# Kernel tuning notes

Measured on AMD Instinct MI355X. Metric: run time of the kernel, lower is better.

Reference implementation:

```python
import jax, jax.numpy as jnp
import numpy as np

EPS = 1e-8
LN_EPS = 1e-5

def _normalize(x):
    # torch F.normalize: x / max(||x||_2, eps)
    n = jnp.linalg.norm(x, axis=-1, keepdims=True)
    return x / jnp.maximum(n, EPS)

def _gelu(x):
    return jax.nn.gelu(x, approximate=False)

def _layernorm(x, g, b):
    mu = jnp.mean(x, axis=-1, keepdims=True)
    var = jnp.var(x, axis=-1, keepdims=True)
    return (x - mu) / jnp.sqrt(var + LN_EPS) * g + b

def setup_inputs() -> dict:
    B, M, N, D = 128, 256, 1024, 256
    key = jax.random.key(0)
    ks = jax.random.split(key, 10)
    def lin(k, fi, fo):
        kw, kb = jax.random.split(k)
        lim = 1.0 / np.sqrt(fi)
        W = jax.random.uniform(kw, (fi, fo), minval=-lim, maxval=lim, dtype=jnp.float32)
        b = jax.random.uniform(kb, (fo,), minval=-lim, maxval=lim, dtype=jnp.float32)
        return W, b
    Wg1, bg1 = lin(ks[0], D, D)
    Wg2, bg2 = lin(ks[1], D, 1)
    Wo1, bo1 = lin(ks[2], 2 * D, D)
    Wo2, bo2 = lin(ks[3], D, D)
    Ws1, bs1 = lin(ks[4], D, D // 2)
    Ws2, bs2 = lin(ks[5], D // 2, 1)
    return {
        "visual_tokens": jax.random.normal(ks[6], (B, N, D), dtype=jnp.float32),
        "text_tokens": jax.random.normal(ks[7], (B, M, D), dtype=jnp.float32),
        "text_mask": jax.random.randint(ks[8], (B, M), 0, 2, dtype=jnp.int32),
        "Wg1": Wg1, "bg1": bg1, "Wg2": Wg2, "bg2": bg2,
        "Wo1": Wo1, "bo1": bo1, "ln_g": jnp.ones((D,), jnp.float32), "ln_b": jnp.zeros((D,), jnp.float32),
        "Wo2": Wo2, "bo2": bo2,
        "Ws1": Ws1, "bs1": bs1, "Ws2": Ws2, "bs2": bs2,
    }

def reference(visual_tokens, text_tokens, text_mask,
              Wg1, bg1, Wg2, bg2, Wo1, bo1, ln_g, ln_b, Wo2, bo2,
              Ws1, bs1, Ws2, bs2):
    vis = _normalize(visual_tokens)   # [B,N,D]
    txt = _normalize(text_tokens)     # [B,M,D]
    sim = jnp.einsum('bmd,bnd->bmn', txt, vis)           # token_patch_sim [B,M,N]
    token_maxsim = jnp.max(sim, axis=-1)                 # [B,M]
    token_best_patch_idx = jnp.argmax(sim, axis=-1)      # [B,M] int
    gathered = jnp.take_along_axis(vis, token_best_patch_idx[..., None], axis=1)  # [B,M,D]
    pair = jnp.concatenate([txt, gathered], axis=-1)     # [B,M,2D]
    # out_proj: Linear -> LayerNorm -> GELU -> Linear
    pair = _gelu(_layernorm(pair @ Wo1 + bo1, ln_g, ln_b)) @ Wo2 + bo2  # [B,M,D]
    # token_gate: Linear -> GELU -> Linear(D,1)
    gate = (_gelu(pair @ Wg1 + bg1) @ Wg2 + bg2)[..., 0]  # [B,M]
    mask = text_mask.astype(sim.dtype)
    token_maxsim = jnp.where(mask == 0, 0.0, token_maxsim)
    gate = jnp.where(mask == 0, -10000.0, gate)
    sim = jnp.where(mask[..., None] == 0, -1.0, sim)
    w = jax.nn.softmax(gate, axis=-1)
    w = w * mask
    w = w / jnp.maximum(jnp.sum(w, axis=-1, keepdims=True), EPS)
    grounding = jnp.sum(pair * w[..., None], axis=1)                   # [B,D]
    contradiction = 1.0 - jnp.sum(token_maxsim * w, axis=-1, keepdims=True)  # [B,1]
    patch_attn = jax.nn.softmax(jnp.swapaxes(sim, 1, 2), axis=-1)      # [B,N,M]
    weighted_patch = jnp.einsum('bnm,bmd->bnd', patch_attn, txt)       # [B,N,D]
    feat = grounding * contradiction + grounding
    score = jax.nn.sigmoid(_gelu(feat @ Ws1 + bs1) @ Ws2 + bs2)        # [B,1]
    pf = jnp.clip(token_maxsim, 0.0, 1.0)
    token_logits = jnp.stack([1.0 - pf, pf], axis=-1)                  # [B,M,2]
    return (sim, token_maxsim, token_best_patch_idx, token_logits,
            grounding, score, weighted_patch)
```

## Files before the change

kernel.cpp:

```cpp
#include <hip/hip_runtime.h>
#include <math.h>

static constexpr int Bc = 128;
static constexpr int Mc = 256;
static constexpr int Nc = 1024;
static constexpr int Dc = 256;

typedef __attribute__((ext_vector_type(8))) short bfrag;
typedef __attribute__((ext_vector_type(4))) float f32x4;

__device__ __forceinline__ float gelu_exact(float x) {
    return 0.5f * x * (1.0f + erff(x * 0.70710678118654752440f));
}

__device__ __forceinline__ unsigned short f2bf_rne(float x) {
    unsigned u = __builtin_bit_cast(unsigned, x);
    unsigned r = u + 0x7fffu + ((u >> 16) & 1u);
    return (unsigned short)(r >> 16);
}
__device__ __forceinline__ unsigned pk2(unsigned short a, unsigned short b) {
    return (unsigned)a | ((unsigned)b << 16);
}

__global__ void normalize_k(const float* __restrict__ vis,
                            const float* __restrict__ txt,
                            unsigned short* __restrict__ vis_b,
                            unsigned short* __restrict__ txt_b,
                            float* __restrict__ invv,
                            float* __restrict__ invt) {
    int wave = (blockIdx.x * blockDim.x + threadIdx.x) >> 6;
    int lane = threadIdx.x & 63;
    const int visRows = Bc * Nc;
    const float* src; unsigned short* dst; float* invp; long long row;
    if (wave < visRows) { src = vis; dst = vis_b; invp = invv; row = wave; }
    else { src = txt; dst = txt_b; invp = invt; row = wave - visRows; }
    float4 v = ((const float4*)(src + row * Dc))[lane];
    float ss = v.x * v.x + v.y * v.y + v.z * v.z + v.w * v.w;
    #pragma unroll
    for (int off = 32; off; off >>= 1) ss += __shfl_xor(ss, off);
    float sc = 1.0f / fmaxf(sqrtf(ss), 1e-8f);
    if (lane == 0) invp[row] = sc;
    unsigned short h0 = f2bf_rne(v.x * sc), h1 = f2bf_rne(v.y * sc);
    unsigned short h2 = f2bf_rne(v.z * sc), h3 = f2bf_rne(v.w * sc);
    *(uint2*)(dst + row * 256 + lane * 4) = make_uint2(pk2(h0, h1), pk2(h2, h3));
}

__global__ __launch_bounds__(256) void tcvt(const float* __restrict__ W,
                                            unsigned short* __restrict__ Wt,
                                            int R, int Cdim) {
    __shared__ unsigned short T[64 * 72];
    int r0 = blockIdx.x * 64, c0 = blockIdx.y * 64;
    int t = threadIdx.x;
    int rl = t >> 4, c4 = (t & 15) << 2;
    #pragma unroll
    for (int i = 0; i < 4; i++) {
        int r = rl + i * 16;
        float4 v = *(const float4*)(W + (long long)(r0 + r) * Cdim + c0 + c4);
        T[(c4 + 0) * 72 + r] = f2bf_rne(v.x);
        T[(c4 + 1) * 72 + r] = f2bf_rne(v.y);
        T[(c4 + 2) * 72 + r] = f2bf_rne(v.z);
        T[(c4 + 3) * 72 + r] = f2bf_rne(v.w);
    }
    __syncthreads();
    #pragma unroll
    for (int i = 0; i < 2; i++) {
        int cc = i * 256 + t, cl = cc >> 3, seg = cc & 7;
        unsigned short sv[8];
        #pragma unroll
        for (int j = 0; j < 8; j++) sv[j] = T[cl * 72 + seg * 8 + j];
        *(uint4*)(Wt + (long long)(c0 + cl) * R + r0 + seg * 8) = *(uint4*)sv;
    }
}

__global__ __launch_bounds__(256) void t_txt(const unsigned short* __restrict__ txt_b,
                                             unsigned short* __restrict__ Tt) {
    __shared__ unsigned short T[64 * 72];
    int b = blockIdx.z;
    int m0 = blockIdx.x * 64, d0 = blockIdx.y * 64;
    const unsigned short* in = txt_b + (long long)b * 256 * 256;
    unsigned short* out = Tt + (long long)b * 256 * 256;
    int t = threadIdx.x;
    #pragma unroll
    for (int i = 0; i < 2; i++) {
        int cc = i * 256 + t, ml = cc >> 3, seg = cc & 7;
        uint4 v = *(const uint4*)(in + (long long)(m0 + ml) * 256 + d0 + seg * 8);
        unsigned short sv[8];
        *(uint4*)sv = v;
        #pragma unroll
        for (int j = 0; j < 8; j++) T[(seg * 8 + j) * 72 + ml] = sv[j];
    }
    __syncthreads();
    #pragma unroll
    for (int i = 0; i < 2; i++) {
        int cc = i * 256 + t, dl = cc >> 3, seg = cc & 7;
        unsigned short sv[8];
        #pragma unroll
        for (int j = 0; j < 8; j++) sv[j] = T[dl * 72 + seg * 8 + j];
        *(uint4*)(out + (long long)(d0 + dl) * 256 + m0 + seg * 8) = *(uint4*)sv;
    }
}

template <int EPI>
__global__ __launch_bounds__(256) void gemm_nt(const unsigned short* __restrict__ A,
                                               const unsigned short* __restrict__ B,
                                               const float* __restrict__ bias,
                                               float* __restrict__ C,
                                               unsigned short* __restrict__ Cs,
                                               int Ks, int lda, int ldb, int ldc,
                                               long long sA, long long sB, long long sC) {
    __shared__ unsigned short As[128 * 64];
    __shared__ unsigned short Bs[128 * 64];
    int z = blockIdx.z;
    const unsigned short* Ab = A + (long long)z * sA + (long long)blockIdx.y * 128 * lda;
    const unsigned short* Bb = B + (long long)z * sB + (long long)blockIdx.x * 128 * ldb;
    int t = threadIdx.x;
    int lane = t & 63, wid = t >> 6;
    int wr = wid >> 1, wc = wid & 1;
    int lr = lane & 15, lk = lane >> 4;
    f32x4 acc[4][4];
    #pragma unroll
    for (int i = 0; i < 4; i++)
        #pragma unroll
        for (int j = 0; j < 4; j++) acc[i][j] = (f32x4){0.f, 0.f, 0.f, 0.f};

    for (int k0 = 0; k0 < Ks; k0 += 64) {
        uint4 va[4], vb[4];
        #pragma unroll
        for (int i = 0; i < 4; i++) {
            int c = i * 256 + t, row = c >> 3, kc = c & 7;
            va[i] = *(const uint4*)(Ab + (long long)row * lda + k0 + kc * 8);
            vb[i] = *(const uint4*)(Bb + (long long)row * ldb + k0 + kc * 8);
        }
        __syncthreads();
        #pragma unroll
        for (int i = 0; i < 4; i++) {
            int c = i * 256 + t, row = c >> 3, kc = c & 7;
            int dst = row * 64 + ((kc ^ (row & 7)) << 3);
            *(uint4*)(As + dst) = va[i];
            *(uint4*)(Bs + dst) = vb[i];
        }
        __syncthreads();
        #pragma unroll
        for (int ks = 0; ks < 2; ks++) {
            bfrag av[4], bv[4];
            #pragma unroll
            for (int f = 0; f < 4; f++) {
                int ra = wr * 64 + f * 16 + lr;
                av[f] = *(const bfrag*)(As + ra * 64 + ((((ks << 2) | lk) ^ (ra & 7)) << 3));
                int rb = wc * 64 + f * 16 + lr;
                bv[f] = *(const bfrag*)(Bs + rb * 64 + ((((ks << 2) | lk) ^ (rb & 7)) << 3));
            }
            #pragma unroll
            for (int fm = 0; fm < 4; fm++)
                #pragma unroll
                for (int fn = 0; fn < 4; fn++)
                    acc[fm][fn] = __builtin_amdgcn_mfma_f32_16x16x32_bf16(av[fm], bv[fn], acc[fm][fn], 0, 0, 0);
        }
    }

    long long cb = (long long)z * sC;
    int rbase = blockIdx.y * 128 + wr * 64;
    int cbase = blockIdx.x * 128 + wc * 64;
    #pragma unroll
    for (int fn = 0; fn < 4; fn++) {
        int col = cbase + fn * 16 + lr;
        float bv_ = (EPI > 0) ? bias[col] : 0.0f;
        #pragma unroll
        for (int fm = 0; fm < 4; fm++) {
            #pragma unroll
            for (int r = 0; r < 4; r++) {
                int row = rbase + fm * 16 + lk * 4 + r;
                float v = acc[fm][fn][r] + bv_;
                if (EPI == 3) v = gelu_exact(v);
                C[cb + (long long)row * ldc + col] = v;
                if (EPI == 2) Cs[(long long)row * ldc + col] = f2bf_rne(v);
            }
        }
    }
}

__global__ void rowstats_kernel(float* __restrict__ sim,
                                const int* __restrict__ mask,
                                const float* __restrict__ txt,
                                const float* __restrict__ vis,
                                const float* __restrict__ invt,
                                const float* __restrict__ invv,
                                float* __restrict__ tms_out,
                                float* __restrict__ idx_out,
                                float* __restrict__ logits_out,
                                int* __restrict__ idx_ws) {
    __shared__ int candS[4][64];
    __shared__ int cntS[4];
    int w = threadIdx.x >> 6, lane = threadIdx.x & 63;
    int row = blockIdx.x * 4 + w;
    float* srow = sim + (long long)row * Nc;
    float4 vals[4];
    float best = -3.0e38f;
    #pragma unroll
    for (int s = 0; s < 4; s++) {
        vals[s] = *(const float4*)(srow + s * 256 + lane * 4);
        best = fmaxf(best, fmaxf(fmaxf(vals[s].x, vals[s].y), fmaxf(vals[s].z, vals[s].w)));
    }
    #pragma unroll
    for (int off = 32; off; off >>= 1) best = fmaxf(best, __shfl_xor(best, off));
    if (lane == 0) cntS[w] = 0;
    __syncthreads();
    float th = best - 4e-3f;
    #pragma unroll
    for (int s = 0; s < 4; s++) {
        int base = s * 256 + lane * 4;
        float4 v = vals[s];
        if (v.x >= th) { int sl = atomicAdd(&cntS[w], 1); if (sl < 64) candS[w][sl] = base; }
        if (v.y >= th) { int sl = atomicAdd(&cntS[w], 1); if (sl < 64) candS[w][sl] = base + 1; }
        if (v.z >= th) { int sl = atomicAdd(&cntS[w], 1); if (sl < 64) candS[w][sl] = base + 2; }
        if (v.w >= th) { int sl = atomicAdd(&cntS[w], 1); if (sl < 64) candS[w][sl] = base + 3; }
    }
    __syncthreads();
    int cnt = min(cntS[w], 64);
    int b = row >> 8;
    int bi = candS[w][0];
    if (cnt > 1) {
        float4 t4 = ((const float4*)(txt + (long long)row * Dc))[lane];
        float it = invt[row];
        float bestv = -3.0e38f; bi = 1 << 30;
        for (int c = 0; c < cnt; c++) {
            int n = candS[w][c];
            float4 v4 = ((const float4*)(vis + ((long long)b * Nc + n) * Dc))[lane];
            float d = t4.x * v4.x + t4.y * v4.y + t4.z * v4.z + t4.w * v4.w;
            #pragma unroll
            for (int off = 32; off; off >>= 1) d += __shfl_xor(d, off);
            float val = d * it * invv[b * Nc + n];
            if (val > bestv || (val == bestv && n < bi)) { bestv = val; bi = n; }
        }
    }
    int mk = mask[row];
    if (lane == 0) {
        float tms = mk ? best : 0.0f;
        tms_out[row] = tms;
        idx_out[row] = (float)bi;
        idx_ws[row] = bi;
        float pf = fminf(fmaxf(tms, 0.0f), 1.0f);
        logits_out[row * 2 + 0] = 1.0f - pf;
        logits_out[row * 2 + 1] = pf;
    }
    if (mk == 0) {
        float4 mv = make_float4(-1.0f, -1.0f, -1.0f, -1.0f);
        #pragma unroll
        for (int s = 0; s < 4; s++) *(float4*)(srow + s * 256 + lane * 4) = mv;
    }
}

__global__ void colstats_kernel(const float* __restrict__ sim,
                                float* __restrict__ cmax,
                                float* __restrict__ crecip) {
    int b = blockIdx.y;
    int n = blockIdx.x * 256 + threadIdx.x;
    const float* base = sim + (long long)b * Mc * Nc + n;
    float mx = -3.0e38f;
    for (int m = 0; m < Mc; m++) mx = fmaxf(mx, base[(long long)m * Nc]);
    float s = 0.0f;
    for (int m = 0; m < Mc; m++) s += expf(base[(long long)m * Nc] - mx);
    cmax[b * Nc + n] = mx;
    crecip[b * Nc + n] = 1.0f / s;
}

__global__ __launch_bounds__(256) void wp_gemm(const float* __restrict__ sim,
                                               const unsigned short* __restrict__ Tt,
                                               const float* __restrict__ cmax,
                                               const float* __restrict__ crecip,
                                               float* __restrict__ wpout) {
    __shared__ unsigned short As[128 * 64];
    __shared__ unsigned short Bs[128 * 64];
    int z = blockIdx.z;
    const float* S = sim + (long long)z * Mc * Nc;
    const unsigned short* Bb = Tt + (long long)z * 256 * 256 + (long long)blockIdx.x * 128 * 256;
    int n0 = blockIdx.y * 128;
    int t = threadIdx.x;
    int lane = t & 63, wid = t >> 6, wr = wid >> 1, wc = wid & 1;
    int lr = lane & 15, lk = lane >> 4;
    int nl = t & 127, mh = t >> 7;
    float cm = cmax[(long long)z * Nc + n0 + nl];
    float cr = crecip[(long long)z * Nc + n0 + nl];
    f32x4 acc[4][4];
    #pragma unroll
    for (int i = 0; i < 4; i++)
        #pragma unroll
        for (int j = 0; j < 4; j++) acc[i][j] = (f32x4){0.f, 0.f, 0.f, 0.f};

    for (int g = 0; g < 4; g++) {
        uint4 vb[4];
        #pragma unroll
        for (int i = 0; i < 4; i++) {
            int c = i * 256 + t, row = c >> 3, kc = c & 7;
            vb[i] = *(const uint4*)(Bb + (long long)row * 256 + g * 64 + kc * 8);
        }
        unsigned short pv[32];
        #pragma unroll
        for (int j = 0; j < 32; j++) {
            int m = g * 64 + mh * 32 + j;
            float v = S[(long long)m * Nc + n0 + nl];
            pv[j] = f2bf_rne(expf(v - cm) * cr);
        }
        __syncthreads();
        #pragma unroll
        for (int i = 0; i < 4; i++) {
            int c = i * 256 + t, row = c >> 3, kc = c & 7;
            *(uint4*)(Bs + row * 64 + ((kc ^ (row & 7)) << 3)) = vb[i];
        }
        #pragma unroll
        for (int q = 0; q < 4; q++) {
            uint4 h = make_uint4(pk2(pv[q * 8 + 0], pv[q * 8 + 1]), pk2(pv[q * 8 + 2], pv[q * 8 + 3]),
                                 pk2(pv[q * 8 + 4], pv[q * 8 + 5]), pk2(pv[q * 8 + 6], pv[q * 8 + 7]));
            *(uint4*)(As + nl * 64 + (((mh * 4 + q) ^ (nl & 7)) << 3)) = h;
        }
        __syncthreads();
        #pragma unroll
        for (int ks = 0; ks < 2; ks++) {
            bfrag av[4], bv2[4];
            #pragma unroll
            for (int f = 0; f < 4; f++) {
                int ra = wr * 64 + f * 16 + lr;
                av[f] = *(const bfrag*)(As + ra * 64 + ((((ks << 2) | lk) ^ (ra & 7)) << 3));
                int rb = wc * 64 + f * 16 + lr;
                bv2[f] = *(const bfrag*)(Bs + rb * 64 + ((((ks << 2) | lk) ^ (rb & 7)) << 3));
            }
            #pragma unroll
            for (int fm = 0; fm < 4; fm++)
                #pragma unroll
                for (int fn = 0; fn < 4; fn++)
                    acc[fm][fn] = __builtin_amdgcn_mfma_f32_16x16x32_bf16(av[fm], bv2[fn], acc[fm][fn], 0, 0, 0);
        }
        __syncthreads();
    }

    float* C = wpout + (long long)z * Nc * Dc;
    int rbase = n0 + wr * 64;
    int cbase = blockIdx.x * 128 + wc * 64;
    #pragma unroll
    for (int fn = 0; fn < 4; fn++) {
        int col = cbase + fn * 16 + lr;
        #pragma unroll
        for (int fm = 0; fm < 4; fm++) {
            #pragma unroll
            for (int r = 0; r < 4; r++) {
                int row = rbase + fm * 16 + lk * 4 + r;
                C[(long long)row * Dc + col] = acc[fm][fn][r];
            }
        }
    }
}

__global__ void gatherpair_k(const unsigned short* __restrict__ txt_b,
                             const unsigned short* __restrict__ vis_b,
                             const int* __restrict__ idx_ws,
                             unsigned short* __restrict__ pair_b) {
    int wave = (blockIdx.x * blockDim.x + threadIdx.x) >> 6;
    int lane = threadIdx.x & 63;
    int b = wave >> 8;
    int bi = idx_ws[wave];
    int half = lane >> 5, c = lane & 31;
    const unsigned short* srcrow = half ? (vis_b + ((long long)b * Nc + bi) * 256)
                                        : (txt_b + (long long)wave * 256);
    uint4 v = *(const uint4*)(srcrow + c * 8);
    *(uint4*)(pair_b + (long long)wave * 512 + half * 256 + c * 8) = v;
}

__global__ void lngelu_k(const float* __restrict__ H,
                         unsigned short* __restrict__ Hb,
                         const float* __restrict__ g,
                         const float* __restrict__ bta) {
    int wave = (blockIdx.x * blockDim.x + threadIdx.x) >> 6;
    int lane = threadIdx.x & 63;
    float4 v = ((const float4*)(H + (long long)wave * Dc))[lane];
    float s = v.x + v.y + v.z + v.w;
    #pragma unroll
    for (int off = 32; off; off >>= 1) s += __shfl_xor(s, off);
    float mu = s * (1.0f / 256.0f);
    float dx = v.x - mu, dy = v.y - mu, dz = v.z - mu, dw = v.w - mu;
    float ss = dx * dx + dy * dy + dz * dz + dw * dw;
    #pragma unroll
    for (int off = 32; off; off >>= 1) ss += __shfl_xor(ss, off);
    float rstd = 1.0f / sqrtf(ss * (1.0f / 256.0f) + 1e-5f);
    float4 G4 = ((const float4*)g)[lane];
    float4 B4 = ((const float4*)bta)[lane];
    unsigned short h0 = f2bf_rne(gelu_exact(dx * rstd * G4.x + B4.x));
    unsigned short h1 = f2bf_rne(gelu_exact(dy * rstd * G4.y + B4.y));
    unsigned short h2 = f2bf_rne(gelu_exact(dz * rstd * G4.z + B4.z));
    unsigned short h3 = f2bf_rne(gelu_exact(dw * rstd * G4.w + B4.w));
    *(uint2*)(Hb + (long long)wave * 256 + lane * 4) = make_uint2(pk2(h0, h1), pk2(h2, h3));
}

__global__ void gate_kernel(const float* __restrict__ G,
                            const float* __restrict__ Wg2,
                            const float* __restrict__ bg2,
                            float* __restrict__ gate) {
    int wave = (blockIdx.x * blockDim.x + threadIdx.x) >> 6;
    int lane = threadIdx.x & 63;
    float4 v = ((const float4*)(G + (long long)wave * Dc))[lane];
    float4 w = ((const float4*)Wg2)[lane];
    float s = v.x * w.x + v.y * w.y + v.z * w.z + v.w * w.w;
    #pragma unroll
    for (int off = 32; off; off >>= 1) s += __shfl_xor(s, off);
    if (lane == 0) gate[wave] = s + bg2[0];
}

__global__ __launch_bounds__(256) void final_kernel(const float* __restrict__ gate,
                                                    const int* __restrict__ mask,
                                                    const float* __restrict__ tms,
                                                    const float* __restrict__ pairO,
                                                    const float* __restrict__ Ws1,
                                                    const float* __restrict__ bs1,
                                                    const float* __restrict__ Ws2,
                                                    const float* __restrict__ bs2,
                                                    float* __restrict__ grounding_out,
                                                    float* __restrict__ score_out) {
    __shared__ float wS[256];
    __shared__ float featS[256];
    __shared__ float hS[128];
    __shared__ float red4[4];
    int b = blockIdx.x, t = threadIdx.x;
    int mk = mask[b * Mc + t];
    float g = mk ? gate[b * Mc + t] : -10000.0f;

    float mx = g;
    #pragma unroll
    for (int off = 32; off; off >>= 1) mx = fmaxf(mx, __shfl_xor(mx, off));
    if ((t & 63) == 0) red4[t >> 6] = mx;
    __syncthreads();
    mx = fmaxf(fmaxf(red4[0], red4[1]), fmaxf(red4[2], red4[3]));
    __syncthreads();

    float e = expf(g - mx);
    float ssum = e;
    #pragma unroll
    for (int off = 32; off; off >>= 1) ssum += __shfl_xor(ssum, off);
    if ((t & 63) == 0) red4[t >> 6] = ssum;
    __syncthreads();
    ssum = red4[0] + red4[1] + red4[2] + red4[3];
    __syncthreads();

    float w = (e / ssum) * (float)mk;
    float s2 = w;
    #pragma unroll
    for (int off = 32; off; off >>= 1) s2 += __shfl_xor(s2, off);
    if ((t & 63) == 0) red4[t >> 6] = s2;
    __syncthreads();
    s2 = red4[0] + red4[1] + red4[2] + red4[3];
    __syncthreads();
    w = w / fmaxf(s2, 1e-8f);
    wS[t] = w;

    float cpart = tms[b * Mc + t] * w;
    #pragma unroll
    for (int off = 32; off; off >>= 1) cpart += __shfl_xor(cpart, off);
    if ((t & 63) == 0) red4[t >> 6] = cpart;
    __syncthreads();
    float contra = 1.0f - (red4[0] + red4[1] + red4[2] + red4[3]);
    __syncthreads();

    const float* P = pairO + (long long)b * Mc * Dc;
    float acc = 0.0f;
    for (int m = 0; m < Mc; m++) acc += wS[m] * P[(long long)m * Dc + t];
    grounding_out[b * Dc + t] = acc;
    featS[t] = acc * (1.0f + contra);
    __syncthreads();

    if (t < 128) {
        float a = bs1[t];
        for (int k = 0; k < Dc; k++) a += featS[k] * Ws1[k * 128 + t];
        hS[t] = gelu_exact(a) * Ws2[t];
    }
    __syncthreads();
    if (t == 0) {
        float sc = bs2[0];
        for (int k = 0; k < 128; k++) sc += hS[k];
        score_out[b] = 1.0f / (1.0f + expf(-sc));
    }
}

extern "C" void kernel_launch(void* const* d_in, const int* in_sizes, int n_in,
                              void* d_out, int out_size, void* d_ws, size_t ws_size,
                              hipStream_t stream) {
    const float* vis  = (const float*)d_in[0];
    const float* txt  = (const float*)d_in[1];
    const int*   mask = (const int*)d_in[2];
    const float* Wg1  = (const float*)d_in[3];
    const float* bg1  = (const float*)d_in[4];
    const float* Wg2  = (const float*)d_in[5];
    const float* bg2  = (const float*)d_in[6];
    const float* Wo1  = (const float*)d_in[7];
    const float* bo1  = (const float*)d_in[8];
    const float* ln_g = (const float*)d_in[9];
    const float* ln_b = (const float*)d_in[10];
    const float* Wo2  = (const float*)d_in[11];
    const float* bo2  = (const float*)d_in[12];
    const float* Ws1  = (const float*)d_in[13];
    const float* bs1  = (const float*)d_in[14];
    const float* Ws2  = (const float*)d_in[15];
    const float* bs2  = (const float*)d_in[16];

    float* out = (float*)d_out;
    float* o_sim    = out;
    float* o_tms    = o_sim + (size_t)Bc * Mc * Nc;
    float* o_idx    = o_tms + (size_t)Bc * Mc;
    float* o_logits = o_idx + (size_t)Bc * Mc;
    float* o_ground = o_logits + (size_t)Bc * Mc * 2;
    float* o_score  = o_ground + (size_t)Bc * Dc;
    float* o_wp     = o_score + (size_t)Bc;

    char* wsb = (char*)d_ws;
    unsigned short* vis_b  = (unsigned short*)(wsb + 0);
    unsigned short* txt_b  = (unsigned short*)(wsb + 67108864);
    unsigned short* Tt     = (unsigned short*)(wsb + 83886080);
    unsigned short* pair_b = (unsigned short*)(wsb + 100663296);
    float*          H1     = (float*)(wsb + 134217728);
    unsigned short* H1_b   = (unsigned short*)(wsb + 167772160);
    float*          pairO  = (float*)(wsb + 184549376);
    unsigned short* pairO_b= (unsigned short*)(wsb + 218103808);
    float*          Gb     = (float*)(wsb + 234881024);
    char* sm = wsb + 268435456;
    float* invv    = (float*)(sm + 0);
    float* invt    = (float*)(sm + 524288);
    float* cmaxb   = (float*)(sm + 655360);
    float* crecipb = (float*)(sm + 1179648);
    int*   idx_ws  = (int*)(sm + 1703936);
    float* gateb   = (float*)(sm + 1835008);
    unsigned short* Wo1_t = (unsigned short*)(sm + 1966080);
    unsigned short* Wo2_t = (unsigned short*)(sm + 2228224);
    unsigned short* Wg1_t = (unsigned short*)(sm + 2359296);

    normalize_k<<<(Bc * Nc + Bc * Mc) / 4, 256, 0, stream>>>(vis, txt, vis_b, txt_b, invv, invt);
    tcvt<<<dim3(8, 4), 256, 0, stream>>>(Wo1, Wo1_t, 512, 256);
    tcvt<<<dim3(4, 4), 256, 0, stream>>>(Wo2, Wo2_t, 256, 256);
    tcvt<<<dim3(4, 4), 256, 0, stream>>>(Wg1, Wg1_t, 256, 256);
    gemm_nt<0><<<dim3(8, 2, 128), 256, 0, stream>>>(txt_b, vis_b, nullptr, o_sim, nullptr,
                                                    256, 256, 256, 1024,
                                                    256LL * 256, 1024LL * 256, 256LL * 1024);
    rowstats_kernel<<<(Bc * Mc) / 4, 256, 0, stream>>>(o_sim, mask, txt, vis, invt, invv,
                                                       o_tms, o_idx, o_logits, idx_ws);
    colstats_kernel<<<dim3(Nc / 256, Bc), 256, 0, stream>>>(o_sim, cmaxb, crecipb);
    t_txt<<<dim3(4, 4, 128), 256, 0, stream>>>(txt_b, Tt);
    wp_gemm<<<dim3(2, 8, 128), 256, 0, stream>>>(o_sim, Tt, cmaxb, crecipb, o_wp);
    gatherpair_k<<<(Bc * Mc) / 4, 256, 0, stream>>>(txt_b, vis_b, idx_ws, pair_b);
    gemm_nt<1><<<dim3(2, 256, 1), 256, 0, stream>>>(pair_b, Wo1_t, bo1, H1, nullptr,
                                                    512, 512, 512, 256, 0, 0, 0);
    lngelu_k<<<(Bc * Mc) / 4, 256, 0, stream>>>(H1, H1_b, ln_g, ln_b);
    gemm_nt<2><<<dim3(2, 256, 1), 256, 0, stream>>>(H1_b, Wo2_t, bo2, pairO, pairO_b,
                                                    256, 256, 256, 256, 0, 0, 0);
    gemm_nt<3><<<dim3(2, 256, 1), 256, 0, stream>>>(pairO_b, Wg1_t, bg1, Gb, nullptr,
                                                    256, 256, 256, 256, 0, 0, 0);
    gate_kernel<<<(Bc * Mc) / 4, 256, 0, stream>>>(Gb, Wg2, bg2, gateb);
    final_kernel<<<Bc, 256, 0, stream>>>(gateb, mask, o_tms, pairO, Ws1, bs1, Ws2, bs2, o_ground, o_score);
}
```

Baseline: 887.5 us.

## Fuse gate projection into GEMM epilogue, use direct-to-LDS loads, restructure stats kernels

Merges the three weight-transpose launches and the gate bias init into one prep kernel. The gate GEMM epilogue now applies GELU, dots with Wg2 and atomically adds into the gate buffer, which removes the Gb intermediate and the gate_kernel pass. GEMM tile loads switch to global_load_lds with swizzled source addresses. Column stats become a single-pass online softmax with float4 loads, wp_gemm covers all 256 output columns per block with 512 threads, and the final kernel runs 512 threads to split its reductions. The atomics make gate summation order nondeterministic.

Result: faster. 753.6 us (-15.1%).

```diff
diff --git a/kernel.cpp b/kernel.cpp
--- a/kernel.cpp
+++ b/kernel.cpp
@@ -20,6 +20,13 @@
 }
 __device__ __forceinline__ unsigned pk2(unsigned short a, unsigned short b) {
     return (unsigned)a | ((unsigned)b << 16);
+}
+
+__device__ __forceinline__ void gld16(const unsigned short* g, unsigned short* l) {
+    __builtin_amdgcn_global_load_lds(
+        (const __attribute__((address_space(1))) unsigned int*)g,
+        (__attribute__((address_space(3))) unsigned int*)l,
+        16, 0, 0);
 }
 
 __global__ void normalize_k(const float* __restrict__ vis,
@@ -45,11 +52,10 @@
     *(uint2*)(dst + row * 256 + lane * 4) = make_uint2(pk2(h0, h1), pk2(h2, h3));
 }
 
-__global__ __launch_bounds__(256) void tcvt(const float* __restrict__ W,
-                                            unsigned short* __restrict__ Wt,
-                                            int R, int Cdim) {
-    __shared__ unsigned short T[64 * 72];
-    int r0 = blockIdx.x * 64, c0 = blockIdx.y * 64;
+__device__ __forceinline__ void tile_tcvt(const float* W, unsigned short* Wt,
+                                          int R, int Cdim, int rt, int ct,
+                                          unsigned short* T) {
+    int r0 = rt * 64, c0 = ct * 64;
     int t = threadIdx.x;
     int rl = t >> 4, c4 = (t & 15) << 2;
     #pragma unroll
@@ -69,6 +75,27 @@
         #pragma unroll
         for (int j = 0; j < 8; j++) sv[j] = T[cl * 72 + seg * 8 + j];
         *(uint4*)(Wt + (long long)(c0 + cl) * R + r0 + seg * 8) = *(uint4*)sv;
+    }
+}
+
+__global__ __launch_bounds__(256) void prep_k(const float* __restrict__ Wo1,
+                                              const float* __restrict__ Wo2,
+                                              const float* __restrict__ Wg1,
+                                              unsigned short* __restrict__ Wo1_t,
+                                              unsigned short* __restrict__ Wo2_t,
+                                              unsigned short* __restrict__ Wg1_t,
+                                              const float* __restrict__ bg2,
+                                              float* __restrict__ gateb) {
+    __shared__ unsigned short T[64 * 72];
+    int job = blockIdx.x;
+    if (job < 32)      tile_tcvt(Wo1, Wo1_t, 512, 256, job >> 2, job & 3, T);
+    else if (job < 48) tile_tcvt(Wo2, Wo2_t, 256, 256, (job - 32) >> 2, (job - 32) & 3, T);
+    else if (job < 64) tile_tcvt(Wg1, Wg1_t, 256, 256, (job - 48) >> 2, (job - 48) & 3, T);
+    else {
+        float v = bg2[0];
+        int base = (job - 64) * 8192 + threadIdx.x;
+        #pragma unroll
+        for (int i = 0; i < 32; i++) gateb[base + i * 256] = v;
     }
 }
 
@@ -106,6 +133,8 @@
                                                const float* __restrict__ bias,
                                                float* __restrict__ C,
                                                unsigned short* __restrict__ Cs,
+                                               const float* __restrict__ wg2,
+                                               float* __restrict__ gateo,
                                                int Ks, int lda, int ldb, int ldc,
                                                long long sA, long long sB, long long sC) {
     __shared__ unsigned short As[128 * 64];
@@ -124,20 +153,15 @@
         for (int j = 0; j < 4; j++) acc[i][j] = (f32x4){0.f, 0.f, 0.f, 0.f};
 
     for (int k0 = 0; k0 < Ks; k0 += 64) {
-        uint4 va[4], vb[4];
+        __syncthreads();
         #pragma unroll
         for (int i = 0; i < 4; i++) {
-            int c = i * 256 + t, row = c >> 3, kc = c & 7;
-            va[i] = *(const uint4*)(Ab + (long long)row * lda + k0 + kc * 8);
-            vb[i] = *(const uint4*)(Bb + (long long)row * ldb + k0 + kc * 8);
-        }
-        __syncthreads();
-        #pragma unroll
-        for (int i = 0; i < 4; i++) {
-            int c = i * 256 + t, row = c >> 3, kc = c & 7;
-            int dst = row * 64 + ((kc ^ (row & 7)) << 3);
-            *(uint4*)(As + dst) = va[i];
-            *(uint4*)(Bs + dst) = vb[i];
+            int wb = i * 256 + (t & 192);
+            int c  = wb + (t & 63);
+            int row = c >> 3, p = c & 7;
+            int sw = (p ^ (row & 7)) << 3;
+            gld16(Ab + (long long)row * lda + k0 + sw, As + wb * 8);
+            gld16(Bb + (long long)row * ldb + k0 + sw, Bs + wb * 8);
         }
         __syncthreads();
         #pragma unroll
@@ -158,22 +182,46 @@
         }
     }
 
-    long long cb = (long long)z * sC;
     int rbase = blockIdx.y * 128 + wr * 64;
     int cbase = blockIdx.x * 128 + wc * 64;
-    #pragma unroll
-    for (int fn = 0; fn < 4; fn++) {
-        int col = cbase + fn * 16 + lr;
-        float bv_ = (EPI > 0) ? bias[col] : 0.0f;
-        #pragma unroll
-        for (int fm = 0; fm < 4; fm++) {
+    if constexpr (EPI == 4) {
+        float part[4][4] = {};
+        #pragma unroll
+        for (int fn = 0; fn < 4; fn++) {
+            int col = cbase + fn * 16 + lr;
+            float bv_ = bias[col];
+            float w2 = wg2[col];
+            #pragma unroll
+            for (int fm = 0; fm < 4; fm++)
+                #pragma unroll
+                for (int r = 0; r < 4; r++)
+                    part[fm][r] += gelu_exact(acc[fm][fn][r] + bv_) * w2;
+        }
+        #pragma unroll
+        for (int fm = 0; fm < 4; fm++)
             #pragma unroll
             for (int r = 0; r < 4; r++) {
-                int row = rbase + fm * 16 + lk * 4 + r;
-                float v = acc[fm][fn][r] + bv_;
-                if (EPI == 3) v = gelu_exact(v);
-                C[cb + (long long)row * ldc + col] = v;
-                if (EPI == 2) Cs[(long long)row * ldc + col] = f2bf_rne(v);
+                float p = part[fm][r];
+                p += __shfl_xor(p, 1); p += __shfl_xor(p, 2);
+                p += __shfl_xor(p, 4); p += __shfl_xor(p, 8);
+                if (lr == 0) atomicAdd(&gateo[rbase + fm * 16 + lk * 4 + r], p);
+            }
+    } else {
+        long long cb = (long long)z * sC;
+        #pragma unroll
+        for (int fn = 0; fn < 4; fn++) {
+            int col = cbase + fn * 16 + lr;
+            float bv_ = (EPI > 0) ? bias[col] : 0.0f;
+            #pragma unroll
+            for (int fm = 0; fm < 4; fm++) {
+                #pragma unroll
+                for (int r = 0; r < 4; r++) {
+                    int row = rbase + fm * 16 + lk * 4 + r;
+                    float v = acc[fm][fn][r] + bv_;
+                    if (EPI == 3) v = gelu_exact(v);
+                    C[cb + (long long)row * ldc + col] = v;
+                    if (EPI == 2) Cs[(long long)row * ldc + col] = f2bf_rne(v);
+                }
             }
         }
     }
@@ -250,33 +298,40 @@
     }
 }
 
-__global__ void colstats_kernel(const float* __restrict__ sim,
-                                float* __restrict__ cmax,
-                                float* __restrict__ crecip) {
+__global__ __launch_bounds__(128) void colstats_kernel(const float* __restrict__ sim,
+                                                       float* __restrict__ cmax,
+                                                       float* __restrict__ crecip) {
     int b = blockIdx.y;
-    int n = blockIdx.x * 256 + threadIdx.x;
-    const float* base = sim + (long long)b * Mc * Nc + n;
-    float mx = -3.0e38f;
-    for (int m = 0; m < Mc; m++) mx = fmaxf(mx, base[(long long)m * Nc]);
-    float s = 0.0f;
-    for (int m = 0; m < Mc; m++) s += expf(base[(long long)m * Nc] - mx);
-    cmax[b * Nc + n] = mx;
-    crecip[b * Nc + n] = 1.0f / s;
-}
-
-__global__ __launch_bounds__(256) void wp_gemm(const float* __restrict__ sim,
+    int n4 = (blockIdx.x * 128 + threadIdx.x) * 4;
+    const float* base = sim + (long long)b * Mc * Nc + n4;
+    float4 mx = make_float4(-3.0e38f, -3.0e38f, -3.0e38f, -3.0e38f);
+    float4 s = make_float4(0.f, 0.f, 0.f, 0.f);
+    for (int m = 0; m < Mc; m++) {
+        float4 v = *(const float4*)(base + (long long)m * Nc);
+        float nm;
+        nm = fmaxf(mx.x, v.x); s.x = s.x * expf(mx.x - nm) + expf(v.x - nm); mx.x = nm;
+        nm = fmaxf(mx.y, v.y); s.y = s.y * expf(mx.y - nm) + expf(v.y - nm); mx.y = nm;
+        nm = fmaxf(mx.z, v.z); s.z = s.z * expf(mx.z - nm) + expf(v.z - nm); mx.z = nm;
+        nm = fmaxf(mx.w, v.w); s.w = s.w * expf(mx.w - nm) + expf(v.w - nm); mx.w = nm;
+    }
+    *(float4*)(cmax + b * Nc + n4) = mx;
+    *(float4*)(crecip + b * Nc + n4) = make_float4(1.f / s.x, 1.f / s.y, 1.f / s.z, 1.f / s.w);
+}
+
+__global__ __launch_bounds__(512) void wp_gemm(const float* __restrict__ sim,
                                                const unsigned short* __restrict__ Tt,
                                                const float* __restrict__ cmax,
                                                const float* __restrict__ crecip,
                                                float* __restrict__ wpout) {
     __shared__ unsigned short As[128 * 64];
-    __shared__ unsigned short Bs[128 * 64];
-    int z = blockIdx.z;
+    __shared__ unsigned short Bs[256 * 64];
+    int z = blockIdx.y;
+    int n0 = blockIdx.x * 128;
     const float* S = sim + (long long)z * Mc * Nc;
-    const unsigned short* Bb = Tt + (long long)z * 256 * 256 + (long long)blockIdx.x * 128 * 256;
-    int n0 = blockIdx.y * 128;
+    const unsigned short* Bb = Tt + (long long)z * 256 * 256;
     int t = threadIdx.x;
-    int lane = t & 63, wid = t >> 6, wr = wid >> 1, wc = wid & 1;
+    int lane = t & 63, wid = t >> 6;
+    int wr = wid >> 2, wc = wid & 3;
     int lr = lane & 15, lk = lane >> 4;
     int nl = t & 127, mh = t >> 7;
     float cm = cmax[(long long)z * Nc + n0 + nl];
@@ -288,30 +343,27 @@
         for (int j = 0; j < 4; j++) acc[i][j] = (f32x4){0.f, 0.f, 0.f, 0.f};
 
     for (int g = 0; g < 4; g++) {
-        uint4 vb[4];
-        #pragma unroll
-        for (int i = 0; i < 4; i++) {
-            int c = i * 256 + t, row = c >> 3, kc = c & 7;
-            vb[i] = *(const uint4*)(Bb + (long long)row * 256 + g * 64 + kc * 8);
-        }
-        unsigned short pv[32];
-        #pragma unroll
-        for (int j = 0; j < 32; j++) {
-            int m = g * 64 + mh * 32 + j;
+        unsigned short pv[16];
+        #pragma unroll
+        for (int j = 0; j < 16; j++) {
+            int m = g * 64 + mh * 16 + j;
             float v = S[(long long)m * Nc + n0 + nl];
             pv[j] = f2bf_rne(expf(v - cm) * cr);
         }
         __syncthreads();
         #pragma unroll
         for (int i = 0; i < 4; i++) {
-            int c = i * 256 + t, row = c >> 3, kc = c & 7;
-            *(uint4*)(Bs + row * 64 + ((kc ^ (row & 7)) << 3)) = vb[i];
-        }
-        #pragma unroll
-        for (int q = 0; q < 4; q++) {
+            int wb = i * 512 + (t & 448);
+            int c  = wb + (t & 63);
+            int row = c >> 3, p = c & 7;
+            gld16(Bb + (long long)row * 256 + g * 64 + ((p ^ (row & 7)) << 3), Bs + wb * 8);
+        }
+        #pragma unroll
+        for (int q = 0; q < 2; q++) {
+            int chunk = mh * 2 + q;
             uint4 h = make_uint4(pk2(pv[q * 8 + 0], pv[q * 8 + 1]), pk2(pv[q * 8 + 2], pv[q * 8 + 3]),
                                  pk2(pv[q * 8 + 4], pv[q * 8 + 5]), pk2(pv[q * 8 + 6], pv[q * 8 + 7]));
-            *(uint4*)(As + nl * 64 + (((mh * 4 + q) ^ (nl & 7)) << 3)) = h;
+            *(uint4*)(As + nl * 64 + ((chunk ^ (nl & 7)) << 3)) = h;
         }
         __syncthreads();
         #pragma unroll
@@ -330,12 +382,11 @@
                 for (int fn = 0; fn < 4; fn++)
                     acc[fm][fn] = __builtin_amdgcn_mfma_f32_16x16x32_bf16(av[fm], bv2[fn], acc[fm][fn], 0, 0, 0);
         }
-        __syncthreads();
     }
 
     float* C = wpout + (long long)z * Nc * Dc;
     int rbase = n0 + wr * 64;
-    int cbase = blockIdx.x * 128 + wc * 64;
+    int cbase = wc * 64;
     #pragma unroll
     for (int fn = 0; fn < 4; fn++) {
         int col = cbase + fn * 16 + lr;
@@ -390,21 +441,7 @@
     *(uint2*)(Hb + (long long)wave * 256 + lane * 4) = make_uint2(pk2(h0, h1), pk2(h2, h3));
 }
 
-__global__ void gate_kernel(const float* __restrict__ G,
-                            const float* __restrict__ Wg2,
-                            const float* __restrict__ bg2,
-                            float* __restrict__ gate) {
-    int wave = (blockIdx.x * blockDim.x + threadIdx.x) >> 6;
-    int lane = threadIdx.x & 63;
-    float4 v = ((const float4*)(G + (long long)wave * Dc))[lane];
-    float4 w = ((const float4*)Wg2)[lane];
-    float s = v.x * w.x + v.y * w.y + v.z * w.z + v.w * w.w;
-    #pragma unroll
-    for (int off = 32; off; off >>= 1) s += __shfl_xor(s, off);
-    if (lane == 0) gate[wave] = s + bg2[0];
-}
-
-__global__ __launch_bounds__(256) void final_kernel(const float* __restrict__ gate,
+__global__ __launch_bounds__(512) void final_kernel(const float* __restrict__ gate,
                                                     const int* __restrict__ mask,
                                                     const float* __restrict__ tms,
                                                     const float* __restrict__ pairO,
@@ -418,63 +455,93 @@
     __shared__ float featS[256];
     __shared__ float hS[128];
     __shared__ float red4[4];
+    __shared__ float gpart[512];
+    __shared__ float hpart[512];
+    __shared__ float contraS;
     int b = blockIdx.x, t = threadIdx.x;
-    int mk = mask[b * Mc + t];
-    float g = mk ? gate[b * Mc + t] : -10000.0f;
-
-    float mx = g;
-    #pragma unroll
-    for (int off = 32; off; off >>= 1) mx = fmaxf(mx, __shfl_xor(mx, off));
-    if ((t & 63) == 0) red4[t >> 6] = mx;
-    __syncthreads();
-    mx = fmaxf(fmaxf(red4[0], red4[1]), fmaxf(red4[2], red4[3]));
-    __syncthreads();
-
-    float e = expf(g - mx);
-    float ssum = e;
-    #pragma unroll
-    for (int off = 32; off; off >>= 1) ssum += __shfl_xor(ssum, off);
-    if ((t & 63) == 0) red4[t >> 6] = ssum;
-    __syncthreads();
-    ssum = red4[0] + red4[1] + red4[2] + red4[3];
-    __syncthreads();
-
-    float w = (e / ssum) * (float)mk;
-    float s2 = w;
-    #pragma unroll
-    for (int off = 32; off; off >>= 1) s2 += __shfl_xor(s2, off);
-    if ((t & 63) == 0) red4[t >> 6] = s2;
-    __syncthreads();
-    s2 = red4[0] + red4[1] + red4[2] + red4[3];
-    __syncthreads();
-    w = w / fmaxf(s2, 1e-8f);
-    wS[t] = w;
-
-    float cpart = tms[b * Mc + t] * w;
-    #pragma unroll
-    for (int off = 32; off; off >>= 1) cpart += __shfl_xor(cpart, off);
-    if ((t & 63) == 0) red4[t >> 6] = cpart;
-    __syncthreads();
-    float contra = 1.0f - (red4[0] + red4[1] + red4[2] + red4[3]);
-    __syncthreads();
-
+    int mk = 0; float g = -10000.0f, tmsv = 0.f;
+    if (t < 256) {
+        mk = mask[b * Mc + t];
+        g = mk ? gate[b * Mc + t] : -10000.0f;
+        tmsv = tms[b * Mc + t];
+    }
+    if (t < 256) {
+        float mx = g;
+        #pragma unroll
+        for (int off = 32; off; off >>= 1) mx = fmaxf(mx, __shfl_xor(mx, off));
+        if ((t & 63) == 0) red4[t >> 6] = mx;
+    }
+    __syncthreads();
+    float mx = fmaxf(fmaxf(red4[0], red4[1]), fmaxf(red4[2], red4[3]));
+    __syncthreads();
+    float e = 0.f;
+    if (t < 256) {
+        e = expf(g - mx);
+        float ssum = e;
+        #pragma unroll
+        for (int off = 32; off; off >>= 1) ssum += __shfl_xor(ssum, off);
+        if ((t & 63) == 0) red4[t >> 6] = ssum;
+    }
+    __syncthreads();
+    float ssum = red4[0] + red4[1] + red4[2] + red4[3];
+    __syncthreads();
+    float w = 0.f;
+    if (t < 256) {
+        w = (e / ssum) * (float)mk;
+        float s2 = w;
+        #pragma unroll
+        for (int off = 32; off; off >>= 1) s2 += __shfl_xor(s2, off);
+        if ((t & 63) == 0) red4[t >> 6] = s2;
+    }
+    __syncthreads();
+    float s2 = red4[0] + red4[1] + red4[2] + red4[3];
+    __syncthreads();
+    if (t < 256) {
+        w = w / fmaxf(s2, 1e-8f);
+        wS[t] = w;
+        float cp = tmsv * w;
+        #pragma unroll
+        for (int off = 32; off; off >>= 1) cp += __shfl_xor(cp, off);
+        if ((t & 63) == 0) red4[t >> 6] = cp;
+    }
+    __syncthreads();
+    if (t == 0) contraS = 1.0f - (red4[0] + red4[1] + red4[2] + red4[3]);
+    __syncthreads();
+
+    int d = t & 255, half = t >> 8;
     const float* P = pairO + (long long)b * Mc * Dc;
     float acc = 0.0f;
-    for (int m = 0; m < Mc; m++) acc += wS[m] * P[(long long)m * Dc + t];
-    grounding_out[b * Dc + t] = acc;
-    featS[t] = acc * (1.0f + contra);
-    __syncthreads();
-
+    for (int i = 0; i < 128; i++) {
+        int m = half * 128 + i;
+        acc += wS[m] * P[(long long)m * Dc + d];
+    }
+    gpart[t] = acc;
+    __syncthreads();
+    if (t < 256) {
+        float s = gpart[t] + gpart[t + 256];
+        grounding_out[b * Dc + t] = s;
+        featS[t] = s * (1.0f + contraS);
+    }
+    __syncthreads();
+
+    int j = t & 127, part = t >> 7;
+    float a = 0.0f;
+    for (int i = 0; i < 64; i++) {
+        int k = part * 64 + i;
+        a += featS[k] * Ws1[k * 128 + j];
+    }
+    hpart[t] = a;
+    __syncthreads();
     if (t < 128) {
-        float a = bs1[t];
-        for (int k = 0; k < Dc; k++) a += featS[k] * Ws1[k * 128 + t];
-        hS[t] = gelu_exact(a) * Ws2[t];
-    }
-    __syncthreads();
-    if (t == 0) {
-        float sc = bs2[0];
-        for (int k = 0; k < 128; k++) sc += hS[k];
-        score_out[b] = 1.0f / (1.0f + expf(-sc));
+        float aa = hpart[t] + hpart[t + 128] + hpart[t + 256] + hpart[t + 384] + bs1[t];
+        hS[t] = gelu_exact(aa) * Ws2[t];
+    }
+    __syncthreads();
+    if (t < 64) {
+        float s = hS[t] + hS[t + 64];
+        #pragma unroll
+        for (int off = 32; off; off >>= 1) s += __shfl_xor(s, off);
+        if (t == 0) score_out[b] = 1.0f / (1.0f + expf(-(s + bs2[0])));
     }
 }
 
@@ -517,8 +584,7 @@
     unsigned short* H1_b   = (unsigned short*)(wsb + 167772160);
     float*          pairO  = (float*)(wsb + 184549376);
     unsigned short* pairO_b= (unsigned short*)(wsb + 218103808);
-    float*          Gb     = (float*)(wsb + 234881024);
-    char* sm = wsb + 268435456;
+    char* sm = wsb + 234881024;
     float* invv    = (float*)(sm + 0);
     float* invt    = (float*)(sm + 524288);
     float* cmaxb   = (float*)(sm + 655360);
@@ -530,25 +596,22 @@
     unsigned short* Wg1_t = (unsigned short*)(sm + 2359296);
 
     normalize_k<<<(Bc * Nc + Bc * Mc) / 4, 256, 0, stream>>>(vis, txt, vis_b, txt_b, invv, invt);
-    tcvt<<<dim3(8, 4), 256, 0, stream>>>(Wo1, Wo1_t, 512, 256);
-    tcvt<<<dim3(4, 4), 256, 0, stream>>>(Wo2, Wo2_t, 256, 256);
-    tcvt<<<dim3(4, 4), 256, 0, stream>>>(Wg1, Wg1_t, 256, 256);
-    gemm_nt<0><<<dim3(8, 2, 128), 256, 0, stream>>>(txt_b, vis_b, nullptr, o_sim, nullptr,
+    prep_k<<<68, 256, 0, stream>>>(Wo1, Wo2, Wg1, Wo1_t, Wo2_t, Wg1_t, bg2, gateb);
+    gemm_nt<0><<<dim3(8, 2, 128), 256, 0, stream>>>(txt_b, vis_b, nullptr, o_sim, nullptr, nullptr, nullptr,
                                                     256, 256, 256, 1024,
                                                     256LL * 256, 1024LL * 256, 256LL * 1024);
     rowstats_kernel<<<(Bc * Mc) / 4, 256, 0, stream>>>(o_sim, mask, txt, vis, invt, invv,
                                                        o_tms, o_idx, o_logits, idx_ws);
-    colstats_kernel<<<dim3(Nc / 256, Bc), 256, 0, stream>>>(o_sim, cmaxb, crecipb);
+    colstats_kernel<<<dim3(2, Bc), 128, 0, stream>>>(o_sim, cmaxb, crecipb);
     t_txt<<<dim3(4, 4, 128), 256, 0, stream>>>(txt_b, Tt);
-    wp_gemm<<<dim3(2, 8, 128), 256, 0, stream>>>(o_sim, Tt, cmaxb, crecipb, o_wp);
+    wp_gemm<<<dim3(8, 128), 512, 0, stream>>>(o_sim, Tt, cmaxb, crecipb, o_wp);
     gatherpair_k<<<(Bc * Mc) / 4, 256, 0, stream>>>(txt_b, vis_b, idx_ws, pair_b);
-    gemm_nt<1><<<dim3(2, 256, 1), 256, 0, stream>>>(pair_b, Wo1_t, bo1, H1, nullptr,
+    gemm_nt<1><<<dim3(2, 256, 1), 256, 0, stream>>>(pair_b, Wo1_t, bo1, H1, nullptr, nullptr, nullptr,
                                                     512, 512, 512, 256, 0, 0, 0);
     lngelu_k<<<(Bc * Mc) / 4, 256, 0, stream>>>(H1, H1_b, ln_g, ln_b);
-    gemm_nt<2><<<dim3(2, 256, 1), 256, 0, stream>>>(H1_b, Wo2_t, bo2, pairO, pairO_b,
+    gemm_nt<2><<<dim3(2, 256, 1), 256, 0, stream>>>(H1_b, Wo2_t, bo2, pairO, pairO_b, nullptr, nullptr,
                                                     256, 256, 256, 256, 0, 0, 0);
-    gemm_nt<3><<<dim3(2, 256, 1), 256, 0, stream>>>(pairO_b, Wg1_t, bg1, Gb, nullptr,
+    gemm_nt<4><<<dim3(2, 256, 1), 256, 0, stream>>>(pairO_b, Wg1_t, bg1, nullptr, nullptr, Wg2, gateb,
                                                     256, 256, 256, 256, 0, 0, 0);
-    gate_kernel<<<(Bc * Mc) / 4, 256, 0, stream>>>(Gb, Wg2, bg2, gateb);
-    final_kernel<<<Bc, 256, 0, stream>>>(gateb, mask, o_tms, pairO, Ws1, bs1, Ws2, bs2, o_ground, o_score);
-}
+    final_kernel<<<Bc, 512, 0, stream>>>(gateb, mask, o_tms, pairO, Ws1, bs1, Ws2, bs2, o_ground, o_score);
+}
```
